# Kernel tuning notes

Measured on AMD Instinct MI355X. Metric: run time of the kernel, lower is better.

The kernel has to match this reference:

```python
import jax, jax.numpy as jnp
import numpy as np

N_HEADS = 16
N_KV_HEADS = 4
HEAD_DIM = 128
D_MODEL = 2048
WINDOW = 1024
THETA = 10000.0
EPS = 1e-6


def _rmsnorm(x, w):
    var = jnp.mean(x * x, axis=-1, keepdims=True)
    return x * jax.lax.rsqrt(var + EPS) * w


def _rope(x, pos):
    # x: [B, H, S, D]; rotate-half (llama-style) RoPE
    d2 = HEAD_DIM // 2
    inv_freq = 1.0 / (THETA ** (jnp.arange(0, HEAD_DIM, 2, dtype=jnp.float32) / HEAD_DIM))
    ang = pos[:, None].astype(jnp.float32) * inv_freq[None, :]  # [S, D/2]
    cos = jnp.cos(ang)[None, None]
    sin = jnp.sin(ang)[None, None]
    x1, x2 = x[..., :d2], x[..., d2:]
    return jnp.concatenate([x1 * cos - x2 * sin, x1 * sin + x2 * cos], axis=-1)


def setup_inputs() -> dict:
    key = jax.random.key(0)
    ks = jax.random.split(key, 7)
    B, S = 1, 2048
    s = 0.02
    return {
        "x": jax.random.normal(ks[0], (B, S, D_MODEL), jnp.float32),
        "wq": jax.random.normal(ks[1], (N_HEADS * HEAD_DIM, D_MODEL), jnp.float32) * s,
        "wk": jax.random.normal(ks[2], (N_KV_HEADS * HEAD_DIM, D_MODEL), jnp.float32) * s,
        "wv": jax.random.normal(ks[3], (N_KV_HEADS * HEAD_DIM, D_MODEL), jnp.float32) * s,
        "wo": jax.random.normal(ks[4], (D_MODEL, N_HEADS * HEAD_DIM), jnp.float32) * s,
        "q_norm_w": jnp.ones((HEAD_DIM,), jnp.float32),
        "k_norm_w": jnp.ones((HEAD_DIM,), jnp.float32),
    }


def reference(x, wq, wk, wv, wo, q_norm_w, k_norm_w):
    B, S, _ = x.shape
    past_length = 0
    scale = HEAD_DIM ** -0.5
    n_rep = N_HEADS // N_KV_HEADS

    q = (x @ wq.T).reshape(B, S, N_HEADS, HEAD_DIM).transpose(0, 2, 1, 3)
    k = (x @ wk.T).reshape(B, S, N_KV_HEADS, HEAD_DIM).transpose(0, 2, 1, 3)
    v = (x @ wv.T).reshape(B, S, N_KV_HEADS, HEAD_DIM).transpose(0, 2, 1, 3)

    q = _rmsnorm(q, q_norm_w)
    k = _rmsnorm(k, k_norm_w)

    pos = jnp.arange(S) + past_length
    q = _rope(q, pos)
    k = _rope(k, pos)

    # GQA: materialize repeated KV heads, as in _repeat_kv
    k_rep = jnp.repeat(k, n_rep, axis=1)  # [B, H, S, D]
    v_rep = jnp.repeat(v, n_rep, axis=1)

    # sliding-window causal mask (total_seq_len=S > WINDOW)
    q_idx = jnp.arange(S)[:, None] + past_length
    k_idx = jnp.arange(S)[None, :]
    mask = (q_idx >= k_idx) & (q_idx - k_idx < WINDOW)  # [S, S]

    scores = jnp.einsum("bhqd,bhkd->bhqk", q, k_rep) * scale
    scores = jnp.where(mask[None, None], scores, jnp.float32(-jnp.inf))
    attn = jax.nn.softmax(scores, axis=-1)
    out = jnp.einsum("bhqk,bhkd->bhqd", attn, v_rep)

    out = out.transpose(0, 2, 1, 3).reshape(B, S, N_HEADS * HEAD_DIM)
    return out @ wo.T
```

## Files before the change

### kernel.cpp

```cpp
#include <hip/hip_runtime.h>
#include <hip/hip_bf16.h>
#include <cstdint>
#include <cstddef>

typedef __attribute__((ext_vector_type(4))) float f32x4;
typedef __attribute__((ext_vector_type(8))) short bf16x8;
typedef __attribute__((ext_vector_type(8))) unsigned short us8;

#define MFMA16(a, b, c) __builtin_amdgcn_mfma_f32_16x16x32_bf16(a, b, c, 0, 0, 0)

__device__ inline unsigned short f2bf(float f) {
    unsigned int u = __float_as_uint(f);
    u += 0x7fffu + ((u >> 16) & 1u);
    return (unsigned short)(u >> 16);
}
__device__ inline float bf2f(unsigned short u) {
    return __uint_as_float((unsigned int)u << 16);
}
__device__ inline unsigned short f2bf_fast(float f) {
    float r;
    asm("v_cvt_pk_bf16_f32 %0, %1, %2" : "=v"(r) : "v"(f), "v"(f));
    return (unsigned short)__float_as_uint(r);
}

__device__ inline void gload_lds16(const void* g, void* l) {
    __builtin_amdgcn_global_load_lds(
        (const __attribute__((address_space(1))) void*)g,
        (__attribute__((address_space(3))) void*)l, 16, 0, 0);
}
__device__ inline unsigned lds_addr(const void* p) {
    return (unsigned)(size_t)((__attribute__((address_space(3))) const void*)p);
}

__global__ __launch_bounds__(256) void prep_all(const float* __restrict__ x,
                                                const float* __restrict__ wq,
                                                const float* __restrict__ wk,
                                                const float* __restrict__ wv,
                                                const float* __restrict__ wo,
                                                unsigned short* __restrict__ xb,
                                                unsigned short* __restrict__ wqkv,
                                                unsigned short* __restrict__ wob,
                                                float2* __restrict__ tbl) {
    const int b = blockIdx.x;
    if (b < 14336) {
        const float* src; unsigned short* dst; int off4;
        if (b < 4096)       { src = x;  dst = xb;                 off4 = b; }
        else if (b < 8192)  { src = wq; dst = wqkv;               off4 = b - 4096; }
        else if (b < 9216)  { src = wk; dst = wqkv + 2048 * 2048; off4 = b - 8192; }
        else if (b < 10240) { src = wv; dst = wqkv + 2560 * 2048; off4 = b - 9216; }
        else                { src = wo; dst = wob;                off4 = b - 10240; }
        int i = (off4 * 256 + threadIdx.x) * 4;
        float4 v = *(const float4*)(src + i);
        ushort4 o;
        o.x = f2bf(v.x); o.y = f2bf(v.y); o.z = f2bf(v.z); o.w = f2bf(v.w);
        *(ushort4*)(dst + i) = o;
    } else {
        int idx = (b - 14336) * 256 + threadIdx.x;
        int row = idx >> 6, t = idx & 63;
        float inv_freq = exp2f((float)t * (-2.0f / 128.0f) * 13.287712379549449f);
        float s, c;
        sincosf((float)row * inv_freq, &s, &c);
        tbl[idx] = make_float2(c, s);
    }
}

__global__ __launch_bounds__(512, 2) void gemm256(const unsigned short* __restrict__ A,
                                                  const unsigned short* __restrict__ B,
                                                  unsigned short* __restrict__ Cp,
                                                  int M, int N, int Kfull, int kspan) {
    __shared__ unsigned short As[3][8192];
    __shared__ unsigned short Bs[3][8192];
    const int tid = threadIdx.x;
    const int lane = tid & 63, wave = tid >> 6;
    const int wr = wave >> 2, wc = wave & 3;
    const int l15 = lane & 15, l4 = lane >> 4;
    const int gx = gridDim.x;
    const int nwg = gx * gridDim.y;
    const int bid0 = blockIdx.y * gx + blockIdx.x;
    const int q8 = nwg >> 3, r8 = nwg & 7;
    const int xcd = bid0 & 7, sub = bid0 >> 3;
    const int wgid = ((xcd < r8) ? xcd * (q8 + 1) : r8 * (q8 + 1) + (xcd - r8) * q8) + sub;
    const int bm = wgid / gx, bn = wgid % gx;
    const int z = blockIdx.z;
    const unsigned short* Az = A + (size_t)z * kspan;
    const unsigned short* Bz = B + (size_t)z * kspan;
    unsigned short* C = Cp + (size_t)z * M * N;
    const int nK = kspan >> 5;

    f32x4 acc[8][4] = {};

    const int r0 = tid >> 2, qs = tid & 3;
    const int qsw = qs ^ ((r0 >> 1) & 3);
    const unsigned short* pa0 = Az + (size_t)(bm * 256 + r0) * Kfull + qsw * 8;
    const unsigned short* pa1 = pa0 + (size_t)128 * Kfull;
    const unsigned short* pb0 = Bz + (size_t)(bn * 256 + r0) * Kfull + qsw * 8;
    const unsigned short* pb1 = pb0 + (size_t)128 * Kfull;

#define STG(kt, bb)                                            \
    do {                                                       \
        gload_lds16(pa0 + (kt) * 32, &As[bb][tid * 8]);        \
        gload_lds16(pa1 + (kt) * 32, &As[bb][4096 + tid * 8]); \
        gload_lds16(pb0 + (kt) * 32, &Bs[bb][tid * 8]);        \
        gload_lds16(pb1 + (kt) * 32, &Bs[bb][4096 + tid * 8]); \
    } while (0)

    const int q = l4 ^ ((l15 >> 1) & 3);
    const unsigned aB = lds_addr(&As[0][0]) + (unsigned)((wr * 128 + l15) * 64 + q * 16);
    const unsigned bB = lds_addr(&Bs[0][0]) + (unsigned)((wc * 64 + l15) * 64 + q * 16);

#define DSR(dst, addr, off) \
    asm volatile("ds_read_b128 %0, %1 offset:" #off : "=v"(dst) : "v"(addr))

    STG(0, 0);
    STG(1, 1);
    int bc = 0, bs = 2;
    for (int kt = 0; kt < nK; ++kt) {
        if (kt + 1 < nK)
            asm volatile("s_waitcnt vmcnt(4)\ns_barrier" ::: "memory");
        else
            asm volatile("s_waitcnt vmcnt(0)\ns_barrier" ::: "memory");
        __builtin_amdgcn_sched_barrier(0);

        bf16x8 a[8], b[4];
        {
            const unsigned aA = aB + bc * 16384;
            const unsigned bA = bB + bc * 16384;
            DSR(a[0], aA, 0);    DSR(a[1], aA, 1024);
            DSR(a[2], aA, 2048); DSR(a[3], aA, 3072);
            DSR(a[4], aA, 4096); DSR(a[5], aA, 5120);
            DSR(a[6], aA, 6144); DSR(a[7], aA, 7168);
            DSR(b[0], bA, 0);    DSR(b[1], bA, 1024);
            DSR(b[2], bA, 2048); DSR(b[3], bA, 3072);
        }
        if (kt + 2 < nK) STG(kt + 2, bs);
        asm volatile("s_waitcnt lgkmcnt(0)" ::: "memory");
        __builtin_amdgcn_sched_barrier(0);

        __builtin_amdgcn_s_setprio(1);
#pragma unroll
        for (int m = 0; m < 8; ++m)
#pragma unroll
            for (int n = 0; n < 4; ++n)
                acc[m][n] = MFMA16(a[m], b[n], acc[m][n]);
        __builtin_amdgcn_s_setprio(0);

        if (++bc == 3) bc = 0;
        if (++bs == 3) bs = 0;
    }
#undef STG
#undef DSR

    for (int m = 0; m < 8; ++m)
        for (int n = 0; n < 4; ++n)
            for (int j = 0; j < 4; ++j) {
                int row = bm * 256 + wr * 128 + m * 16 + l4 * 4 + j;
                int col = bn * 256 + wc * 64 + n * 16 + l15;
                C[(size_t)row * N + col] = f2bf_fast(acc[m][n][j]);
            }
}

__global__ __launch_bounds__(256) void norm_rope(const unsigned short* __restrict__ p0,
                                                 const unsigned short* __restrict__ p1,
                                                 const float* __restrict__ qw,
                                                 const float* __restrict__ kw,
                                                 const float2* __restrict__ tbl,
                                                 unsigned short* __restrict__ Qb,
                                                 unsigned short* __restrict__ Kb) {
    const int row = blockIdx.x;
    const int head = blockIdx.y * 4 + (threadIdx.x >> 6);
    const int t = threadIdx.x & 63;
    const size_t off = (size_t)row * 3072 + head * 128;
    float x1 = bf2f(p0[off + t]) + bf2f(p1[off + t]);
    float x2 = bf2f(p0[off + t + 64]) + bf2f(p1[off + t + 64]);
    float ss = x1 * x1 + x2 * x2;
    for (int m = 32; m; m >>= 1) ss += __shfl_xor(ss, m);
    float r = rsqrtf(ss * (1.0f / 128.0f) + 1e-6f);
    const float* w = (head < 16) ? qw : kw;
    float y1 = x1 * r * w[t], y2 = x2 * r * w[t + 64];
    float2 cs = tbl[row * 64 + t];
    x1 = y1 * cs.x - y2 * cs.y;
    x2 = y1 * cs.y + y2 * cs.x;
    if (head < 16) {
        const float SCALE2 = 0.12751879526654698f;
        x1 *= SCALE2; x2 *= SCALE2;
    }
    unsigned short* dst = (head < 16) ? Qb + ((size_t)head * 2048 + row) * 128
                                      : Kb + ((size_t)(head - 16) * 2048 + row) * 128;
    dst[t] = f2bf(x1);
    dst[t + 64] = f2bf(x2);
}

__global__ __launch_bounds__(256) void transpose_v(const unsigned short* __restrict__ p0,
                                                   const unsigned short* __restrict__ p1,
                                                   unsigned short* __restrict__ VbT) {
    const int kt = blockIdx.x;
    const int h  = blockIdx.y;
    __shared__ unsigned short T[64 * 132];
    const int tid = threadIdx.x;
    for (int i = 0; i < 8; ++i) {
        int s = i * 256 + tid;
        int r = s >> 5, c = (s & 31) * 4;
        size_t off = (size_t)(kt * 64 + r) * 3072 + (20 + h) * 128 + c;
        ushort4 a = *(const ushort4*)(p0 + off);
        ushort4 b = *(const ushort4*)(p1 + off);
        ushort4 o;
        o.x = f2bf(bf2f(a.x) + bf2f(b.x));
        o.y = f2bf(bf2f(a.y) + bf2f(b.y));
        o.z = f2bf(bf2f(a.z) + bf2f(b.z));
        o.w = f2bf(bf2f(a.w) + bf2f(b.w));
        *(ushort4*)&T[r * 132 + c] = o;
    }
    __syncthreads();
    for (int i = 0; i < 4; ++i) {
        int s = i * 256 + tid;
        int d = s >> 3, ck = (s & 7) * 8;
        us8 v;
        for (int j = 0; j < 8; ++j) {
            int c = ck + j;
            int k = (c & 3) * 16 + (c >> 2);
            v[j] = T[k * 132 + d];
        }
        *(us8*)(VbT + (size_t)h * 128 * 2048 + (size_t)d * 2048 + kt * 64 + ck) = v;
    }
}

__global__ __launch_bounds__(512) void attn_fwd(const unsigned short* __restrict__ Qb,
                                                const unsigned short* __restrict__ Kb,
                                                const unsigned short* __restrict__ VbT,
                                                unsigned short* __restrict__ Ob) {
    const int bid = blockIdx.x;
    const int p = bid & 7;
    const int qt = bid >> 3;
    const int q0 = qt * 64;
    __shared__ unsigned short Ks[2][64 * 128];
    __shared__ unsigned short Vs[128 * 64];
    __shared__ unsigned short Ps[8][16 * 68];
    const int tid = threadIdx.x;
    const int lane = tid & 63, wave = tid >> 6;
    const int l15 = lane & 15, l4 = lane >> 4;
    const int h = 2 * p + (wave >> 2);
    const int rgrp = wave & 3;
    const int kvh = p >> 1;

    bf16x8 qf[4];
    {
        const unsigned short* qrow =
            Qb + ((size_t)h * 2048 + q0 + rgrp * 16 + l15) * 128 + l4 * 8;
        for (int kk = 0; kk < 4; ++kk) qf[kk] = *(const bf16x8*)(qrow + kk * 32);
    }
    f32x4 o[8] = {};
    float m2[4], lp[4];
    for (int j = 0; j < 4; ++j) { m2[j] = -1e30f; lp[j] = 0.0f; }
    const int kt_lo = (qt >= 16) ? (qt - 16) : 0;

    const unsigned short* Kh = Kb + (size_t)kvh * 2048 * 128;
    const unsigned short* Vh = VbT + (size_t)kvh * 128 * 2048;

    int ksr[2], ksc[2], vsr[2], vsc[2];
    for (int i = 0; i < 2; ++i) {
        int s = i * 512 + tid;
        ksr[i] = s >> 4;
        ksc[i] = (((s & 15) * 16) ^ ((ksr[i] & 7) << 4)) >> 1;
        vsr[i] = s >> 3;
        vsc[i] = (((s & 7) * 16) ^ ((vsr[i] & 7) << 4)) >> 1;
    }

    for (int i = 0; i < 2; ++i)
        gload_lds16(Kh + (size_t)(kt_lo * 64 + ksr[i]) * 128 + ksc[i],
                    &Ks[0][(i * 512 + tid) * 8]);

    int cur = 0;
    for (int kt = kt_lo; kt <= qt; ++kt) {
        asm volatile("s_waitcnt vmcnt(0)\ns_barrier" ::: "memory");
        __builtin_amdgcn_sched_barrier(0);

        for (int i = 0; i < 2; ++i)
            gload_lds16(Vh + (size_t)vsr[i] * 2048 + kt * 64 + vsc[i],
                        &Vs[(i * 512 + tid) * 8]);
        if (kt < qt) {
            for (int i = 0; i < 2; ++i)
                gload_lds16(Kh + (size_t)((kt + 1) * 64 + ksr[i]) * 128 + ksc[i],
                            &Ks[cur ^ 1][(i * 512 + tid) * 8]);
        }

        f32x4 s[4] = {};
        __builtin_amdgcn_s_setprio(1);
        for (int nn = 0; nn < 4; ++nn)
            for (int kk = 0; kk < 4; ++kk) {
                int r = nn * 16 + l15;
                int cb = (kk * 64 + l4 * 16) ^ ((r & 7) << 4);
                bf16x8 kf = *(const bf16x8*)((const char*)&Ks[cur][0] + r * 256 + cb);
                s[nn] = MFMA16(qf[kk], kf, s[nn]);
            }
        __builtin_amdgcn_s_setprio(0);

        float pv4[4][4];
        const bool masked = (kt == qt) || (qt >= 16 && kt == kt_lo);
        if (masked) {
            for (int nn = 0; nn < 4; ++nn) {
                int kc = kt * 64 + nn * 16 + l15;
                for (int j = 0; j < 4; ++j) {
                    int qr = q0 + rgrp * 16 + l4 * 4 + j;
                    unsigned diff = (unsigned)(qr - kc);
                    pv4[nn][j] = (diff < 1024u) ? s[nn][j] : -1e30f;
                }
            }
        } else {
            for (int nn = 0; nn < 4; ++nn)
                for (int j = 0; j < 4; ++j) pv4[nn][j] = s[nn][j];
        }

        float mxl[4];
        bool flag = true;
        for (int j = 0; j < 4; ++j) {
            mxl[j] = fmaxf(fmaxf(pv4[0][j], pv4[1][j]), fmaxf(pv4[2][j], pv4[3][j]));
            flag = flag && (mxl[j] <= m2[j] + 11.0f);
        }
        if (!__all(flag)) {
            for (int j = 0; j < 4; ++j) {
                float mx = mxl[j];
                for (int mk = 8; mk; mk >>= 1) mx = fmaxf(mx, __shfl_xor(mx, mk));
                float mnew = fmaxf(m2[j], mx);
                float corr = exp2f(m2[j] - mnew);
                m2[j] = mnew;
                lp[j] *= corr;
                for (int dd = 0; dd < 8; ++dd) o[dd][j] *= corr;
            }
        }
        for (int j = 0; j < 4; ++j) {
            float rs = 0.0f;
            for (int nn = 0; nn < 4; ++nn) {
                float pv = exp2f(pv4[nn][j] - m2[j]);
                pv4[nn][j] = pv;
                rs += pv;
            }
            lp[j] += rs;
        }

        for (int j = 0; j < 4; ++j) {
            int row = l4 * 4 + j;
            unsigned lo, hi;
            asm("v_cvt_pk_bf16_f32 %0, %1, %2" : "=v"(lo) : "v"(pv4[0][j]), "v"(pv4[1][j]));
            asm("v_cvt_pk_bf16_f32 %0, %1, %2" : "=v"(hi) : "v"(pv4[2][j]), "v"(pv4[3][j]));
            int cb = (l15 * 8) ^ ((row & 7) << 4);
            *(uint2*)((char*)&Ps[wave][0] + row * 136 + cb) = make_uint2(lo, hi);
        }

        bf16x8 pa[2];
        for (int kk2 = 0; kk2 < 2; ++kk2) {
            int cb = (kk2 * 64 + l4 * 16) ^ ((l15 & 7) << 4);
            pa[kk2] = *(const bf16x8*)((const char*)&Ps[wave][0] + l15 * 136 + cb);
        }

        if (kt < qt)
            asm volatile("s_waitcnt vmcnt(2)\ns_barrier" ::: "memory");
        else
            asm volatile("s_waitcnt vmcnt(0)\ns_barrier" ::: "memory");
        __builtin_amdgcn_sched_barrier(0);

        __builtin_amdgcn_s_setprio(1);
        for (int dd = 0; dd < 8; ++dd)
            for (int kk2 = 0; kk2 < 2; ++kk2) {
                int d = dd * 16 + l15;
                int cb = (kk2 * 64 + l4 * 16) ^ ((d & 7) << 4);
                bf16x8 vf = *(const bf16x8*)((const char*)&Vs[0] + d * 128 + cb);
                o[dd] = MFMA16(pa[kk2], vf, o[dd]);
            }
        __builtin_amdgcn_s_setprio(0);
        cur ^= 1;
    }

    for (int j = 0; j < 4; ++j) {
        float lt = lp[j];
        for (int mk = 8; mk; mk >>= 1) lt += __shfl_xor(lt, mk);
        float inv = 1.0f / lt;
        int row = q0 + rgrp * 16 + l4 * 4 + j;
        unsigned short* orow = Ob + (size_t)row * 2048 + h * 128;
        for (int dd = 0; dd < 8; ++dd) orow[dd * 16 + l15] = f2bf_fast(o[dd][j] * inv);
    }
}

__global__ __launch_bounds__(256) void add4(const unsigned short* __restrict__ p,
                                            float* __restrict__ out, int n) {
    int i = (blockIdx.x * 256 + threadIdx.x) * 8;
    if (i >= n) return;
    us8 a = *(const us8*)(p + i);
    us8 b = *(const us8*)(p + 4194304 + i);
    us8 c = *(const us8*)(p + 8388608 + i);
    us8 d = *(const us8*)(p + 12582912 + i);
    f32x4 o0, o1;
    for (int j = 0; j < 4; ++j)
        o0[j] = (bf2f(a[j]) + bf2f(b[j])) + (bf2f(c[j]) + bf2f(d[j]));
    for (int j = 0; j < 4; ++j)
        o1[j] = (bf2f(a[j + 4]) + bf2f(b[j + 4])) + (bf2f(c[j + 4]) + bf2f(d[j + 4]));
    *(f32x4*)(out + i) = o0;
    *(f32x4*)(out + i + 4) = o1;
}

extern "C" void kernel_launch(void* const* d_in, const int* in_sizes, int n_in,
                              void* d_out, int out_size, void* d_ws, size_t ws_size,
                              hipStream_t stream) {
    const float* x  = (const float*)d_in[0];
    const float* wq = (const float*)d_in[1];
    const float* wk = (const float*)d_in[2];
    const float* wv = (const float*)d_in[3];
    const float* wo = (const float*)d_in[4];
    const float* qw = (const float*)d_in[5];
    const float* kw = (const float*)d_in[6];
    float* out = (float*)d_out;

    char* ws = (char*)d_ws;
    unsigned short* xb   = (unsigned short*)(ws + 0);
    unsigned short* wqkv = (unsigned short*)(ws + 8388608);
    unsigned short* wob  = (unsigned short*)(ws + 20971520);
    unsigned short* qkvP = (unsigned short*)(ws + 29360128);
    unsigned short* Qb   = (unsigned short*)(ws + 54525952);
    unsigned short* Kb   = (unsigned short*)(ws + 62914560);
    unsigned short* VbT  = (unsigned short*)(ws + 65011712);
    unsigned short* Ob   = (unsigned short*)(ws + 67108864);
    unsigned short* outP = (unsigned short*)(ws + 29360128);
    float2*         tbl  = (float2*)(ws + 104857600);

    prep_all<<<dim3(14848), dim3(256), 0, stream>>>(x, wq, wk, wv, wo, xb, wqkv, wob, tbl);
    gemm256<<<dim3(12, 8, 2), dim3(512), 0, stream>>>(xb, wqkv, qkvP, 2048, 3072, 2048, 1024);
    norm_rope<<<dim3(2048, 5), dim3(256), 0, stream>>>(qkvP, qkvP + 2048 * 3072, qw, kw, tbl, Qb, Kb);
    transpose_v<<<dim3(32, 4), dim3(256), 0, stream>>>(qkvP, qkvP + 2048 * 3072, VbT);
    attn_fwd<<<dim3(256), dim3(512), 0, stream>>>(Qb, Kb, VbT, Ob);
    gemm256<<<dim3(8, 8, 4), dim3(512), 0, stream>>>(Ob, wob, outP, 2048, 2048, 2048, 512);
    add4<<<dim3(2048), dim3(256), 0, stream>>>(outP, out, 2048 * 2048);
}
```

Before: 126.5 us.

## Double-buffer V tiles and prefetch them with K to drop mid-iteration barrier

V tiles now get their own double buffer in shared memory and are prefetched one iteration ahead together with the next K tile. This removes the second wait-and-barrier inside each attention iteration, which previously stalled the PV MFMAs until the current V load arrived. In exchange, LDS use per block rises by 16 KB, which may reduce occupancy, and the loop now has only one barrier per iteration.

```diff
diff --git a/kernel.cpp b/kernel.cpp
--- a/kernel.cpp
+++ b/kernel.cpp
@@ -233,8 +233,8 @@
     const int qt = bid >> 3;
     const int q0 = qt * 64;
     __shared__ unsigned short Ks[2][64 * 128];
-    __shared__ unsigned short Vs[128 * 64];
-    __shared__ unsigned short Ps[8][16 * 68];
+    __shared__ unsigned short Vs[2][128 * 64];
+    __shared__ char PsB[8][16 * 136];
     const int tid = threadIdx.x;
     const int lane = tid & 63, wave = tid >> 6;
     const int l15 = lane & 15, l4 = lane >> 4;
@@ -265,22 +265,26 @@
         vsc[i] = (((s & 7) * 16) ^ ((vsr[i] & 7) << 4)) >> 1;
     }
 
-    for (int i = 0; i < 2; ++i)
+    for (int i = 0; i < 2; ++i) {
         gload_lds16(Kh + (size_t)(kt_lo * 64 + ksr[i]) * 128 + ksc[i],
                     &Ks[0][(i * 512 + tid) * 8]);
+        gload_lds16(Vh + (size_t)vsr[i] * 2048 + kt_lo * 64 + vsc[i],
+                    &Vs[0][(i * 512 + tid) * 8]);
+    }
 
     int cur = 0;
     for (int kt = kt_lo; kt <= qt; ++kt) {
         asm volatile("s_waitcnt vmcnt(0)\ns_barrier" ::: "memory");
         __builtin_amdgcn_sched_barrier(0);
 
-        for (int i = 0; i < 2; ++i)
-            gload_lds16(Vh + (size_t)vsr[i] * 2048 + kt * 64 + vsc[i],
-                        &Vs[(i * 512 + tid) * 8]);
         if (kt < qt) {
-            for (int i = 0; i < 2; ++i)
-                gload_lds16(Kh + (size_t)((kt + 1) * 64 + ksr[i]) * 128 + ksc[i],
+            const int kn = kt + 1;
+            for (int i = 0; i < 2; ++i) {
+                gload_lds16(Kh + (size_t)(kn * 64 + ksr[i]) * 128 + ksc[i],
                             &Ks[cur ^ 1][(i * 512 + tid) * 8]);
+                gload_lds16(Vh + (size_t)vsr[i] * 2048 + kn * 64 + vsc[i],
+                            &Vs[cur ^ 1][(i * 512 + tid) * 8]);
+            }
         }
 
         f32x4 s[4] = {};
@@ -343,27 +347,21 @@
             asm("v_cvt_pk_bf16_f32 %0, %1, %2" : "=v"(lo) : "v"(pv4[0][j]), "v"(pv4[1][j]));
             asm("v_cvt_pk_bf16_f32 %0, %1, %2" : "=v"(hi) : "v"(pv4[2][j]), "v"(pv4[3][j]));
             int cb = (l15 * 8) ^ ((row & 7) << 4);
-            *(uint2*)((char*)&Ps[wave][0] + row * 136 + cb) = make_uint2(lo, hi);
+            *(uint2*)(&PsB[wave][0] + row * 136 + cb) = make_uint2(lo, hi);
         }
 
         bf16x8 pa[2];
         for (int kk2 = 0; kk2 < 2; ++kk2) {
             int cb = (kk2 * 64 + l4 * 16) ^ ((l15 & 7) << 4);
-            pa[kk2] = *(const bf16x8*)((const char*)&Ps[wave][0] + l15 * 136 + cb);
-        }
-
-        if (kt < qt)
-            asm volatile("s_waitcnt vmcnt(2)\ns_barrier" ::: "memory");
-        else
-            asm volatile("s_waitcnt vmcnt(0)\ns_barrier" ::: "memory");
-        __builtin_amdgcn_sched_barrier(0);
+            pa[kk2] = *(const bf16x8*)(&PsB[wave][0] + l15 * 136 + cb);
+        }
 
         __builtin_amdgcn_s_setprio(1);
         for (int dd = 0; dd < 8; ++dd)
             for (int kk2 = 0; kk2 < 2; ++kk2) {
                 int d = dd * 16 + l15;
                 int cb = (kk2 * 64 + l4 * 16) ^ ((d & 7) << 4);
-                bf16x8 vf = *(const bf16x8*)((const char*)&Vs[0] + d * 128 + cb);
+                bf16x8 vf = *(const bf16x8*)((const char*)&Vs[cur][0] + d * 128 + cb);
                 o[dd] = MFMA16(pa[kk2], vf, o[dd]);
             }
         __builtin_amdgcn_s_setprio(0);
```

After: 131.5 us. 1.04x slower.

## Split attention key range across two blocks and merge partials in combine kernel

Applied to the files above, without the earlier changes.

Each query tile's key-tile range is split into two halves processed by separate blocks, doubling the grid, and each half writes an unnormalized-then-normalized partial output plus its row max and sum. A new combine kernel rescales and merges the two partials into the final output. The V tile is also double-buffered. This targets load imbalance and low parallelism from long causal/sliding-window chains, at the cost of extra memory traffic for partials, an extra launch, and more LDS per block.

```diff
diff --git a/kernel.cpp b/kernel.cpp
--- a/kernel.cpp
+++ b/kernel.cpp
@@ -227,14 +227,17 @@
 __global__ __launch_bounds__(512) void attn_fwd(const unsigned short* __restrict__ Qb,
                                                 const unsigned short* __restrict__ Kb,
                                                 const unsigned short* __restrict__ VbT,
-                                                unsigned short* __restrict__ Ob) {
+                                                unsigned short* __restrict__ On,
+                                                float2* __restrict__ Ml) {
     const int bid = blockIdx.x;
     const int p = bid & 7;
-    const int qt = bid >> 3;
+    const int j2 = bid >> 3;
+    const int qt = j2 >> 1;
+    const int half = j2 & 1;
     const int q0 = qt * 64;
     __shared__ unsigned short Ks[2][64 * 128];
-    __shared__ unsigned short Vs[128 * 64];
-    __shared__ unsigned short Ps[8][16 * 68];
+    __shared__ unsigned short Vs[2][128 * 64];
+    __shared__ char PsB[8][16 * 136];
     const int tid = threadIdx.x;
     const int lane = tid & 63, wave = tid >> 6;
     const int l15 = lane & 15, l4 = lane >> 4;
@@ -251,7 +254,12 @@
     f32x4 o[8] = {};
     float m2[4], lp[4];
     for (int j = 0; j < 4; ++j) { m2[j] = -1e30f; lp[j] = 0.0f; }
+
     const int kt_lo = (qt >= 16) ? (qt - 16) : 0;
+    const int n = qt - kt_lo + 1;
+    const int n0 = n >> 1;
+    const int my_lo = half ? kt_lo + n0 : kt_lo;
+    const int my_hi = half ? qt : kt_lo + n0 - 1;
 
     const unsigned short* Kh = Kb + (size_t)kvh * 2048 * 128;
     const unsigned short* Vh = VbT + (size_t)kvh * 128 * 2048;
@@ -265,119 +273,145 @@
         vsc[i] = (((s & 7) * 16) ^ ((vsr[i] & 7) << 4)) >> 1;
     }
 
-    for (int i = 0; i < 2; ++i)
-        gload_lds16(Kh + (size_t)(kt_lo * 64 + ksr[i]) * 128 + ksc[i],
-                    &Ks[0][(i * 512 + tid) * 8]);
-
-    int cur = 0;
-    for (int kt = kt_lo; kt <= qt; ++kt) {
-        asm volatile("s_waitcnt vmcnt(0)\ns_barrier" ::: "memory");
-        __builtin_amdgcn_sched_barrier(0);
-
+    if (my_lo <= my_hi) {
         for (int i = 0; i < 2; ++i)
-            gload_lds16(Vh + (size_t)vsr[i] * 2048 + kt * 64 + vsc[i],
-                        &Vs[(i * 512 + tid) * 8]);
-        if (kt < qt) {
+            gload_lds16(Kh + (size_t)(my_lo * 64 + ksr[i]) * 128 + ksc[i],
+                        &Ks[0][(i * 512 + tid) * 8]);
+
+        int cur = 0;
+        for (int kt = my_lo; kt <= my_hi; ++kt) {
+            asm volatile("s_waitcnt vmcnt(0)\ns_barrier" ::: "memory");
+            __builtin_amdgcn_sched_barrier(0);
+
             for (int i = 0; i < 2; ++i)
-                gload_lds16(Kh + (size_t)((kt + 1) * 64 + ksr[i]) * 128 + ksc[i],
-                            &Ks[cur ^ 1][(i * 512 + tid) * 8]);
+                gload_lds16(Vh + (size_t)vsr[i] * 2048 + kt * 64 + vsc[i],
+                            &Vs[cur][(i * 512 + tid) * 8]);
+            if (kt < my_hi) {
+                for (int i = 0; i < 2; ++i)
+                    gload_lds16(Kh + (size_t)((kt + 1) * 64 + ksr[i]) * 128 + ksc[i],
+                                &Ks[cur ^ 1][(i * 512 + tid) * 8]);
+            }
+
+            f32x4 s[4] = {};
+            __builtin_amdgcn_s_setprio(1);
+            for (int nn = 0; nn < 4; ++nn)
+                for (int kk = 0; kk < 4; ++kk) {
+                    int r = nn * 16 + l15;
+                    int cb = (kk * 64 + l4 * 16) ^ ((r & 7) << 4);
+                    bf16x8 kf = *(const bf16x8*)((const char*)&Ks[cur][0] + r * 256 + cb);
+                    s[nn] = MFMA16(qf[kk], kf, s[nn]);
+                }
+            __builtin_amdgcn_s_setprio(0);
+
+            float pv4[4][4];
+            const bool masked = (kt == qt) || (qt >= 16 && kt == kt_lo);
+            if (masked) {
+                for (int nn = 0; nn < 4; ++nn) {
+                    int kc = kt * 64 + nn * 16 + l15;
+                    for (int j = 0; j < 4; ++j) {
+                        int qr = q0 + rgrp * 16 + l4 * 4 + j;
+                        unsigned diff = (unsigned)(qr - kc);
+                        pv4[nn][j] = (diff < 1024u) ? s[nn][j] : -1e30f;
+                    }
+                }
+            } else {
+                for (int nn = 0; nn < 4; ++nn)
+                    for (int j = 0; j < 4; ++j) pv4[nn][j] = s[nn][j];
+            }
+
+            float mxl[4];
+            bool flag = true;
+            for (int j = 0; j < 4; ++j) {
+                mxl[j] = fmaxf(fmaxf(pv4[0][j], pv4[1][j]), fmaxf(pv4[2][j], pv4[3][j]));
+                flag = flag && (mxl[j] <= m2[j] + 11.0f);
+            }
+            if (!__all(flag)) {
+                for (int j = 0; j < 4; ++j) {
+                    float mx = mxl[j];
+                    for (int mk = 8; mk; mk >>= 1) mx = fmaxf(mx, __shfl_xor(mx, mk));
+                    float mnew = fmaxf(m2[j], mx);
+                    float corr = exp2f(m2[j] - mnew);
+                    m2[j] = mnew;
+                    lp[j] *= corr;
+                    for (int dd = 0; dd < 8; ++dd) o[dd][j] *= corr;
+                }
+            }
+            for (int j = 0; j < 4; ++j) {
+                float rs = 0.0f;
+                for (int nn = 0; nn < 4; ++nn) {
+                    float pv = exp2f(pv4[nn][j] - m2[j]);
+                    pv4[nn][j] = pv;
+                    rs += pv;
+                }
+                lp[j] += rs;
+            }
+
+            for (int j = 0; j < 4; ++j) {
+                int row = l4 * 4 + j;
+                unsigned lo, hi;
+                asm("v_cvt_pk_bf16_f32 %0, %1, %2" : "=v"(lo) : "v"(pv4[0][j]), "v"(pv4[1][j]));
+                asm("v_cvt_pk_bf16_f32 %0, %1, %2" : "=v"(hi) : "v"(pv4[2][j]), "v"(pv4[3][j]));
+                int cb = (l15 * 8) ^ ((row & 7) << 4);
+                *(uint2*)(&PsB[wave][0] + row * 136 + cb) = make_uint2(lo, hi);
+            }
+
+            bf16x8 pa[2];
+            for (int kk2 = 0; kk2 < 2; ++kk2) {
+                int cb = (kk2 * 64 + l4 * 16) ^ ((l15 & 7) << 4);
+                pa[kk2] = *(const bf16x8*)(&PsB[wave][0] + l15 * 136 + cb);
+            }
+
+            if (kt < my_hi)
+                asm volatile("s_waitcnt vmcnt(2)\ns_barrier" ::: "memory");
+            else
+                asm volatile("s_waitcnt vmcnt(0)\ns_barrier" ::: "memory");
+            __builtin_amdgcn_sched_barrier(0);
+
+            __builtin_amdgcn_s_setprio(1);
+            for (int dd = 0; dd < 8; ++dd)
+                for (int kk2 = 0; kk2 < 2; ++kk2) {
+                    int d = dd * 16 + l15;
+                    int cb = (kk2 * 64 + l4 * 16) ^ ((d & 7) << 4);
+                    bf16x8 vf = *(const bf16x8*)((const char*)&Vs[cur][0] + d * 128 + cb);
+                    o[dd] = MFMA16(pa[kk2], vf, o[dd]);
+                }
+            __builtin_amdgcn_s_setprio(0);
+            cur ^= 1;
         }
-
-        f32x4 s[4] = {};
-        __builtin_amdgcn_s_setprio(1);
-        for (int nn = 0; nn < 4; ++nn)
-            for (int kk = 0; kk < 4; ++kk) {
-                int r = nn * 16 + l15;
-                int cb = (kk * 64 + l4 * 16) ^ ((r & 7) << 4);
-                bf16x8 kf = *(const bf16x8*)((const char*)&Ks[cur][0] + r * 256 + cb);
-                s[nn] = MFMA16(qf[kk], kf, s[nn]);
-            }
-        __builtin_amdgcn_s_setprio(0);
-
-        float pv4[4][4];
-        const bool masked = (kt == qt) || (qt >= 16 && kt == kt_lo);
-        if (masked) {
-            for (int nn = 0; nn < 4; ++nn) {
-                int kc = kt * 64 + nn * 16 + l15;
-                for (int j = 0; j < 4; ++j) {
-                    int qr = q0 + rgrp * 16 + l4 * 4 + j;
-                    unsigned diff = (unsigned)(qr - kc);
-                    pv4[nn][j] = (diff < 1024u) ? s[nn][j] : -1e30f;
-                }
-            }
-        } else {
-            for (int nn = 0; nn < 4; ++nn)
-                for (int j = 0; j < 4; ++j) pv4[nn][j] = s[nn][j];
-        }
-
-        float mxl[4];
-        bool flag = true;
-        for (int j = 0; j < 4; ++j) {
-            mxl[j] = fmaxf(fmaxf(pv4[0][j], pv4[1][j]), fmaxf(pv4[2][j], pv4[3][j]));
-            flag = flag && (mxl[j] <= m2[j] + 11.0f);
-        }
-        if (!__all(flag)) {
-            for (int j = 0; j < 4; ++j) {
-                float mx = mxl[j];
-                for (int mk = 8; mk; mk >>= 1) mx = fmaxf(mx, __shfl_xor(mx, mk));
-                float mnew = fmaxf(m2[j], mx);
-                float corr = exp2f(m2[j] - mnew);
-                m2[j] = mnew;
-                lp[j] *= corr;
-                for (int dd = 0; dd < 8; ++dd) o[dd][j] *= corr;
-            }
-        }
-        for (int j = 0; j < 4; ++j) {
-            float rs = 0.0f;
-            for (int nn = 0; nn < 4; ++nn) {
-                float pv = exp2f(pv4[nn][j] - m2[j]);
-                pv4[nn][j] = pv;
-                rs += pv;
-            }
-            lp[j] += rs;
-        }
-
-        for (int j = 0; j < 4; ++j) {
-            int row = l4 * 4 + j;
-            unsigned lo, hi;
-            asm("v_cvt_pk_bf16_f32 %0, %1, %2" : "=v"(lo) : "v"(pv4[0][j]), "v"(pv4[1][j]));
-            asm("v_cvt_pk_bf16_f32 %0, %1, %2" : "=v"(hi) : "v"(pv4[2][j]), "v"(pv4[3][j]));
-            int cb = (l15 * 8) ^ ((row & 7) << 4);
-            *(uint2*)((char*)&Ps[wave][0] + row * 136 + cb) = make_uint2(lo, hi);
-        }
-
-        bf16x8 pa[2];
-        for (int kk2 = 0; kk2 < 2; ++kk2) {
-            int cb = (kk2 * 64 + l4 * 16) ^ ((l15 & 7) << 4);
-            pa[kk2] = *(const bf16x8*)((const char*)&Ps[wave][0] + l15 * 136 + cb);
-        }
-
-        if (kt < qt)
-            asm volatile("s_waitcnt vmcnt(2)\ns_barrier" ::: "memory");
-        else
-            asm volatile("s_waitcnt vmcnt(0)\ns_barrier" ::: "memory");
-        __builtin_amdgcn_sched_barrier(0);
-
-        __builtin_amdgcn_s_setprio(1);
-        for (int dd = 0; dd < 8; ++dd)
-            for (int kk2 = 0; kk2 < 2; ++kk2) {
-                int d = dd * 16 + l15;
-                int cb = (kk2 * 64 + l4 * 16) ^ ((d & 7) << 4);
-                bf16x8 vf = *(const bf16x8*)((const char*)&Vs[0] + d * 128 + cb);
-                o[dd] = MFMA16(pa[kk2], vf, o[dd]);
-            }
-        __builtin_amdgcn_s_setprio(0);
-        cur ^= 1;
     }
 
     for (int j = 0; j < 4; ++j) {
         float lt = lp[j];
         for (int mk = 8; mk; mk >>= 1) lt += __shfl_xor(lt, mk);
-        float inv = 1.0f / lt;
+        float inv = (lt > 0.0f) ? 1.0f / lt : 0.0f;
         int row = q0 + rgrp * 16 + l4 * 4 + j;
-        unsigned short* orow = Ob + (size_t)row * 2048 + h * 128;
+        unsigned short* orow = On + (((size_t)half * 16 + h) * 2048 + row) * 128;
         for (int dd = 0; dd < 8; ++dd) orow[dd * 16 + l15] = f2bf_fast(o[dd][j] * inv);
-    }
+        if (l15 == 0)
+            Ml[((size_t)half * 16 + h) * 2048 + row] = make_float2(m2[j], lt);
+    }
+}
+
+__global__ __launch_bounds__(256) void attn_combine(const unsigned short* __restrict__ On,
+                                                    const float2* __restrict__ Ml,
+                                                    unsigned short* __restrict__ Ob) {
+    int idx = blockIdx.x * 4 + (threadIdx.x >> 6);
+    int h = idx >> 11, row = idx & 2047;
+    int lane = threadIdx.x & 63;
+    const unsigned short* n0 = On + ((size_t)h * 2048 + row) * 128;
+    const unsigned short* n1 = On + ((size_t)(16 + h) * 2048 + row) * 128;
+    float2 ml0 = Ml[(size_t)h * 2048 + row];
+    float2 ml1 = Ml[(size_t)(16 + h) * 2048 + row];
+    float m = fmaxf(ml0.x, ml1.x);
+    float w0 = ml0.y * exp2f(ml0.x - m);
+    float w1 = ml1.y * exp2f(ml1.x - m);
+    float inv = 1.0f / (w0 + w1);
+    unsigned a = *(const unsigned*)(n0 + lane * 2);
+    unsigned b = *(const unsigned*)(n1 + lane * 2);
+    float o0 = bf2f((unsigned short)a) * w0 + bf2f((unsigned short)b) * w1;
+    float o1 = bf2f((unsigned short)(a >> 16)) * w0 + bf2f((unsigned short)(b >> 16)) * w1;
+    unsigned r0 = f2bf_fast(o0 * inv), r1 = f2bf_fast(o1 * inv);
+    *(unsigned*)(Ob + (size_t)row * 2048 + h * 128 + lane * 2) = r0 | (r1 << 16);
 }
 
 __global__ __launch_bounds__(256) void add4(const unsigned short* __restrict__ p,
@@ -418,6 +452,8 @@
     unsigned short* Kb   = (unsigned short*)(ws + 62914560);
     unsigned short* VbT  = (unsigned short*)(ws + 65011712);
     unsigned short* Ob   = (unsigned short*)(ws + 67108864);
+    unsigned short* OnB  = (unsigned short*)(ws + 75497472);
+    float2*         MlB  = (float2*)(ws + 92274688);
     unsigned short* outP = (unsigned short*)(ws + 29360128);
     float2*         tbl  = (float2*)(ws + 104857600);
 
@@ -425,7 +461,8 @@
     gemm256<<<dim3(12, 8, 2), dim3(512), 0, stream>>>(xb, wqkv, qkvP, 2048, 3072, 2048, 1024);
     norm_rope<<<dim3(2048, 5), dim3(256), 0, stream>>>(qkvP, qkvP + 2048 * 3072, qw, kw, tbl, Qb, Kb);
     transpose_v<<<dim3(32, 4), dim3(256), 0, stream>>>(qkvP, qkvP + 2048 * 3072, VbT);
-    attn_fwd<<<dim3(256), dim3(512), 0, stream>>>(Qb, Kb, VbT, Ob);
+    attn_fwd<<<dim3(512), dim3(512), 0, stream>>>(Qb, Kb, VbT, OnB, MlB);
+    attn_combine<<<dim3(8192), dim3(256), 0, stream>>>(OnB, MlB, Ob);
     gemm256<<<dim3(8, 8, 4), dim3(512), 0, stream>>>(Ob, wob, outP, 2048, 2048, 2048, 512);
     add4<<<dim3(2048), dim3(256), 0, stream>>>(outP, out, 2048 * 2048);
 }
```

After: 141.1 us. 1.12x slower.
